# Kernel tuning notes

Measured on AMD Instinct MI355X. Metric: run time of the kernel, lower is better.

The kernel has to match this reference:

```python
import jax, jax.numpy as jnp
import numpy as np

MAX_PATH_DISTANCE = 5


def setup_inputs() -> dict:
    key = jax.random.key(0)
    k1, k2, k3, k4, k5 = jax.random.split(key, 5)
    N = 8192
    E = 4_000_000
    x = jax.random.normal(k1, (N, 128), dtype=jnp.float32)
    src = jax.random.randint(k2, (E,), 0, N, dtype=jnp.int64)
    dst = jax.random.randint(k3, (E,), 0, N, dtype=jnp.int64)
    # path lengths; original computes len(paths[src][dst]) >= 1
    path_len = jax.random.randint(k4, (E,), 0, 6, dtype=jnp.int64)
    # learned parameter b of shape [max_path_distance]
    b = jax.random.normal(k5, (MAX_PATH_DISTANCE,), dtype=jnp.float32)
    return {"x": x, "b": b, "src": src, "dst": dst, "path_len": path_len}


def reference(x, b, src, dst, path_len):
    N = x.shape[0]
    # index = min(len, max_path_distance) - 1, clamped to valid range
    idx = jnp.clip(path_len, 1, MAX_PATH_DISTANCE) - 1  # [E]
    vals = b[idx]  # [E] gather from tiny table
    spatial = jnp.zeros((N, N), dtype=b.dtype)
    spatial = spatial.at[src, dst].set(vals)  # scatter into pairwise bias matrix
    return spatial
```

## Files before the change

kernel.cpp:

```cpp
#include <hip/hip_runtime.h>

#define MAX_PATH_DISTANCE 5
#define NROW 8192
#define ROWS_PER_BKT 128
#define NBKT 64
#define SLICES 17
#define EPB 4096
#define CAPB (SLICES * EPB)
#define CAPR 768
#define BLK 512
#define NWAVE 8
#define NHG 4
#define EPT 8


__device__ __forceinline__ int clamp_bidx(int pl) {
    int c = pl < 1 ? 1 : (pl > MAX_PATH_DISTANCE ? MAX_PATH_DISTANCE : pl);
    return c - 1;
}

__global__ __launch_bounds__(BLK) void se_coarse(
        const int4* __restrict__ src4, const int4* __restrict__ dst4,
        const int4* __restrict__ plen4,
        unsigned long long* __restrict__ bkt,
        unsigned int* __restrict__ bkt_cur, int E4) {
    __shared__ __align__(16) unsigned long long stage[EPB];
    __shared__ unsigned int hist[NWAVE][NBKT], wb[NWAVE][NBKT];
    __shared__ unsigned int base_l[NBKT], gbase[NBKT], s_total;
    const int tid = threadIdx.x;
    const int w   = tid >> 6;
    const int q0  = blockIdx.x * (EPB / 4);

    for (int i = tid; i < NWAVE * NBKT; i += BLK) (&hist[0][0])[i] = 0u;
    __syncthreads();

    unsigned long long ent[EPT];
#pragma unroll
    for (int g = 0; g < 2; ++g) {
        int q = q0 + g * BLK + tid;
        if (q < E4) {
            int4 s = src4[q], d = dst4[q], p = plen4[q];
            int ss[4] = {s.x, s.y, s.z, s.w};
            int dd[4] = {d.x, d.y, d.z, d.w};
            int pp[4] = {p.x, p.y, p.z, p.w};
#pragma unroll
            for (int c = 0; c < 4; ++c) {
                int e = (q << 2) + c;
                unsigned int key = ((unsigned int)(e + 1) << 3)
                                 | (unsigned int)clamp_bidx(pp[c]);
                unsigned long long v =
                      ((unsigned long long)(unsigned int)ss[c] << 38)
                    | ((unsigned long long)(unsigned int)dd[c] << 25)
                    | (unsigned long long)key;
                ent[g * 4 + c] = v;
                atomicAdd(&hist[w][(unsigned int)(v >> 45)], 1u);
            }
        } else {
#pragma unroll
            for (int c = 0; c < 4; ++c) ent[g * 4 + c] = 0ull;
        }
    }
    __syncthreads();

    if (tid < NBKT) {
        unsigned int t = 0;
#pragma unroll
        for (int ww = 0; ww < NWAVE; ++ww) t += hist[ww][tid];
        base_l[tid] = t;
    }
    __syncthreads();
    if (tid == 0) {
        unsigned int run = 0;
        for (int i = 0; i < NBKT; ++i) {
            unsigned int t = base_l[i]; base_l[i] = run; run += t;
        }
        s_total = run;
    }
    __syncthreads();
    if (tid < NBKT) {
        unsigned int t = base_l[tid], tot = 0;
#pragma unroll
        for (int ww = 0; ww < NWAVE; ++ww) {
            wb[ww][tid] = t; t += hist[ww][tid]; tot += hist[ww][tid];
        }
        gbase[tid] = atomicAdd(&bkt_cur[tid], tot);
    }
    __syncthreads();

#pragma unroll
    for (int j = 0; j < EPT; ++j) {
        if (ent[j]) {
            unsigned int bb = (unsigned int)(ent[j] >> 45);
            unsigned int p  = atomicAdd(&wb[w][bb], 1u);
            stage[p] = ent[j];
        }
    }
    __syncthreads();

    const unsigned int total = s_total;
    for (unsigned int i = tid; i < total; i += BLK) {
        unsigned long long v = stage[i];
        unsigned int bb  = (unsigned int)(v >> 45);
        unsigned int pos = gbase[bb] + (i - base_l[bb]);
        if (pos < CAPB) bkt[(size_t)bb * CAPB + pos] = v;
    }
}

__global__ __launch_bounds__(BLK) void se_fine(
        const unsigned long long* __restrict__ bkt,
        const unsigned int* __restrict__ bkt_cur,
        unsigned long long* __restrict__ rbins,
        unsigned int* __restrict__ rcur) {
    __shared__ __align__(16) unsigned long long stage[EPB];
    __shared__ unsigned int hist[NHG][ROWS_PER_BKT];
    __shared__ unsigned int wb[NHG][ROWS_PER_BKT];
    __shared__ unsigned int base_l[ROWS_PER_BKT], gbase[ROWS_PER_BKT], s_total;
    const int tid = threadIdx.x;
    const int w   = tid >> 7;
    const int b   = blockIdx.x / SLICES;
    const int sl  = blockIdx.x % SLICES;

    unsigned int cnt = bkt_cur[b]; if (cnt > CAPB) cnt = CAPB;
    const int i0 = sl * EPB;
    int n = (int)cnt - i0;
    if (n <= 0) return;
    if (n > EPB) n = EPB;

    for (int i = tid; i < NHG * ROWS_PER_BKT; i += BLK) (&hist[0][0])[i] = 0u;
    __syncthreads();

    const unsigned long long* bp = bkt + (size_t)b * CAPB + i0;
    unsigned long long ent[EPT];
#pragma unroll
    for (int j = 0; j < EPT; ++j) {
        int i = j * BLK + tid;
        ent[j] = 0ull;
        if (i < n) {
            ent[j] = bp[i];
            atomicAdd(&hist[w][(unsigned int)(ent[j] >> 38) & 127u], 1u);
        }
    }
    __syncthreads();

    if (tid < ROWS_PER_BKT) {
        unsigned int t = 0;
#pragma unroll
        for (int ww = 0; ww < NHG; ++ww) t += hist[ww][tid];
        base_l[tid] = t;
    }
    __syncthreads();
    if (tid == 0) {
        unsigned int run = 0;
        for (int i = 0; i < ROWS_PER_BKT; ++i) {
            unsigned int t = base_l[i]; base_l[i] = run; run += t;
        }
        s_total = run;
    }
    __syncthreads();
    if (tid < ROWS_PER_BKT) {
        unsigned int t = base_l[tid], tot = 0;
#pragma unroll
        for (int ww = 0; ww < NHG; ++ww) {
            wb[ww][tid] = t; t += hist[ww][tid]; tot += hist[ww][tid];
        }
        gbase[tid] = atomicAdd(&rcur[b * ROWS_PER_BKT + tid], tot);
    }
    __syncthreads();

#pragma unroll
    for (int j = 0; j < EPT; ++j) {
        if (ent[j]) {
            unsigned int rl = (unsigned int)(ent[j] >> 38) & 127u;
            unsigned int p  = atomicAdd(&wb[w][rl], 1u);
            stage[p] = ent[j];
        }
    }
    __syncthreads();

    const unsigned int total = s_total;
    for (unsigned int i = tid; i < total; i += BLK) {
        unsigned long long v = stage[i];
        unsigned int s   = (unsigned int)((v >> 38) & 0x1FFFu);
        unsigned int rl  = s & 127u;
        unsigned int pos = gbase[rl] + (i - base_l[rl]);
        if (pos < CAPR) rbins[(size_t)s * CAPR + pos] = v;
    }
}

__global__ __launch_bounds__(BLK) void se_rows(
        const unsigned long long* __restrict__ rbins,
        const unsigned int* __restrict__ rcur,
        const float* __restrict__ bias,
        float* __restrict__ out) {
    __shared__ unsigned int lds[NROW];
    const int tid = threadIdx.x;
    const int r0  = blockIdx.x * 2;

    unsigned int cntA = rcur[r0];     if (cntA > CAPR) cntA = CAPR;
    unsigned int cntB = rcur[r0 + 1]; if (cntB > CAPR) cntB = CAPR;
    const unsigned long long* bpA = rbins + (size_t)r0 * CAPR;
    const unsigned long long* bpB = bpA + CAPR;

    unsigned long long a0 = 0ull, a1 = 0ull, b0 = 0ull, b1 = 0ull;
    if ((unsigned int)tid < cntA)        a0 = bpA[tid];
    if ((unsigned int)tid + BLK < cntA)  a1 = bpA[tid + BLK];
    if ((unsigned int)tid < cntB)        b0 = bpB[tid];
    if ((unsigned int)tid + BLK < cntB)  b1 = bpB[tid + BLK];

    for (int i = tid; i < NROW; i += BLK) lds[i] = 0u;
    __syncthreads();
    if (a0) atomicMax(&lds[(unsigned int)((a0 >> 25) & 0x1FFFu)],
                      (unsigned int)(a0 & 0x1FFFFFFu));
    if (a1) atomicMax(&lds[(unsigned int)((a1 >> 25) & 0x1FFFu)],
                      (unsigned int)(a1 & 0x1FFFFFFu));
    __syncthreads();
    if (a0) {
        unsigned int key = (unsigned int)(a0 & 0x1FFFFFFu);
        unsigned int d   = (unsigned int)((a0 >> 25) & 0x1FFFu);
        if (lds[d] == key) lds[d] = __float_as_uint(bias[key & 7u]);
    }
    if (a1) {
        unsigned int key = (unsigned int)(a1 & 0x1FFFFFFu);
        unsigned int d   = (unsigned int)((a1 >> 25) & 0x1FFFu);
        if (lds[d] == key) lds[d] = __float_as_uint(bias[key & 7u]);
    }
    __syncthreads();
    {
        float4* out4 = reinterpret_cast<float4*>(out + (size_t)r0 * NROW);
        const float4* l4 = reinterpret_cast<const float4*>(lds);
#pragma unroll
        for (int k = 0; k < NROW / 4 / BLK; ++k)
            out4[k * BLK + tid] = l4[k * BLK + tid];
    }
    __syncthreads();

    for (int i = tid; i < NROW; i += BLK) lds[i] = 0u;
    __syncthreads();
    if (b0) atomicMax(&lds[(unsigned int)((b0 >> 25) & 0x1FFFu)],
                      (unsigned int)(b0 & 0x1FFFFFFu));
    if (b1) atomicMax(&lds[(unsigned int)((b1 >> 25) & 0x1FFFu)],
                      (unsigned int)(b1 & 0x1FFFFFFu));
    __syncthreads();
    if (b0) {
        unsigned int key = (unsigned int)(b0 & 0x1FFFFFFu);
        unsigned int d   = (unsigned int)((b0 >> 25) & 0x1FFFu);
        if (lds[d] == key) lds[d] = __float_as_uint(bias[key & 7u]);
    }
    if (b1) {
        unsigned int key = (unsigned int)(b1 & 0x1FFFFFFu);
        unsigned int d   = (unsigned int)((b1 >> 25) & 0x1FFFu);
        if (lds[d] == key) lds[d] = __float_as_uint(bias[key & 7u]);
    }
    __syncthreads();
    {
        float4* out4 = reinterpret_cast<float4*>(out + (size_t)(r0 + 1) * NROW);
        const float4* l4 = reinterpret_cast<const float4*>(lds);
#pragma unroll
        for (int k = 0; k < NROW / 4 / BLK; ++k)
            out4[k * BLK + tid] = l4[k * BLK + tid];
    }
}


__global__ void se_scatter_keys(const int* __restrict__ src,
                                const int* __restrict__ dst,
                                const int* __restrict__ plen,
                                unsigned int* __restrict__ out,
                                int E, int N) {
    int e = blockIdx.x * blockDim.x + threadIdx.x;
    if (e >= E) return;
    unsigned int key = ((unsigned int)(e + 1) << 3)
                     | (unsigned int)clamp_bidx(plen[e]);
    atomicMax(&out[(size_t)src[e] * (size_t)N + (size_t)dst[e]], key);
}

__global__ void se_resolve(const int* __restrict__ src,
                           const int* __restrict__ dst,
                           const int* __restrict__ plen,
                           const float* __restrict__ b,
                           unsigned int* __restrict__ out,
                           int E, int N) {
    int e = blockIdx.x * blockDim.x + threadIdx.x;
    if (e >= E) return;
    unsigned int key = ((unsigned int)(e + 1) << 3)
                     | (unsigned int)clamp_bidx(plen[e]);
    size_t off = (size_t)src[e] * (size_t)N + (size_t)dst[e];
    if (out[off] == key) {
        reinterpret_cast<float*>(out)[off] = b[key & 7u];
    }
}


extern "C" void kernel_launch(void* const* d_in, const int* in_sizes, int n_in,
                              void* d_out, int out_size, void* d_ws, size_t ws_size,
                              hipStream_t stream) {
    const float* b    = (const float*)d_in[1];
    const int*   src  = (const int*)d_in[2];
    const int*   dst  = (const int*)d_in[3];
    const int*   plen = (const int*)d_in[4];

    const int N = in_sizes[0] / 128;
    const int E = in_sizes[2];

    const size_t rbins_bytes = (size_t)NROW * CAPR * sizeof(unsigned long long);
    const size_t bkt_bytes   = (size_t)NBKT * CAPB * sizeof(unsigned long long);
    const size_t cur_bytes   = (size_t)(NROW + NBKT) * sizeof(unsigned int);
    const size_t need = rbins_bytes + bkt_bytes + cur_bytes;

    if (N == NROW && (unsigned int)E < (1u << 22) && (E % 4) == 0 &&
        ws_size >= need) {
        unsigned long long* rbins = (unsigned long long*)d_ws;
        unsigned long long* bktp  = (unsigned long long*)((char*)d_ws + rbins_bytes);
        unsigned int* rcur = (unsigned int*)((char*)d_ws + rbins_bytes + bkt_bytes);
        unsigned int* bcur = rcur + NROW;

        hipMemsetAsync(rcur, 0, cur_bytes, stream);
        se_coarse<<<(E + EPB - 1) / EPB, BLK, 0, stream>>>(
            (const int4*)src, (const int4*)dst, (const int4*)plen,
            bktp, bcur, E / 4);
        se_fine<<<NBKT * SLICES, BLK, 0, stream>>>(bktp, bcur, rbins, rcur);
        se_rows<<<NROW / 2, BLK, 0, stream>>>(rbins, rcur, b, (float*)d_out);
    } else {
        const int block = 256;
        const int gridE = (E + block - 1) / block;
        hipMemsetAsync(d_out, 0, (size_t)out_size * sizeof(float), stream);
        se_scatter_keys<<<gridE, block, 0, stream>>>(src, dst, plen,
                                                     (unsigned int*)d_out, E, N);
        se_resolve<<<gridE, block, 0, stream>>>(src, dst, plen, b,
                                                (unsigned int*)d_out, E, N);
    }
}
```

Baseline: 107.9 us.

## Replace LDS atomic histograms with wave-level ballot match ranking and shuffle scans

In both the coarse and fine bucketing kernels, per-element LDS atomicAdds for the histogram and the scatter pass are replaced by a ballot-based match: lanes in a wave with the same bucket are grouped, ranked by popcount, and one leader lane updates the per-wave counter. The single-thread serial prefix sum over buckets becomes a wave shuffle scan. The fine kernel moves from 4 to 8 per-wave histogram groups. This removes LDS atomic contention and a serial scan, but adds 6–7 ballots per element, which could cost more when buckets rarely match within a wave.

```diff
diff --git a/kernel.cpp b/kernel.cpp
--- a/kernel.cpp
+++ b/kernel.cpp
@@ -10,13 +10,24 @@
 #define CAPR 768
 #define BLK 512
 #define NWAVE 8
-#define NHG 4
 #define EPT 8
 
 
 __device__ __forceinline__ int clamp_bidx(int pl) {
     int c = pl < 1 ? 1 : (pl > MAX_PATH_DISTANCE ? MAX_PATH_DISTANCE : pl);
     return c - 1;
+}
+
+template <int NBITS>
+__device__ __forceinline__ unsigned long long same_mask(unsigned int b,
+                                                        unsigned long long valid) {
+    unsigned long long same = valid;
+#pragma unroll
+    for (int k = 0; k < NBITS; ++k) {
+        unsigned long long m = __ballot((b >> k) & 1u);
+        same &= ((b >> k) & 1u) ? m : ~m;
+    }
+    return same;
 }
 
 __global__ __launch_bounds__(BLK) void se_coarse(
@@ -25,11 +36,14 @@
         unsigned long long* __restrict__ bkt,
         unsigned int* __restrict__ bkt_cur, int E4) {
     __shared__ __align__(16) unsigned long long stage[EPB];
-    __shared__ unsigned int hist[NWAVE][NBKT], wb[NWAVE][NBKT];
-    __shared__ unsigned int base_l[NBKT], gbase[NBKT], s_total;
-    const int tid = threadIdx.x;
-    const int w   = tid >> 6;
-    const int q0  = blockIdx.x * (EPB / 4);
+    __shared__ unsigned int hist[NWAVE][NBKT];
+    __shared__ unsigned int base_l[NBKT], cnt_col[NBKT], gbase[NBKT];
+    __shared__ unsigned int s_total;
+    const int tid  = threadIdx.x;
+    const int w    = tid >> 6;
+    const int lane = tid & 63;
+    const unsigned long long lane_lt = ((unsigned long long)1 << lane) - 1ull;
+    const int q0 = blockIdx.x * (EPB / 4);
 
     for (int i = tid; i < NWAVE * NBKT; i += BLK) (&hist[0][0])[i] = 0u;
     __syncthreads();
@@ -48,51 +62,70 @@
                 int e = (q << 2) + c;
                 unsigned int key = ((unsigned int)(e + 1) << 3)
                                  | (unsigned int)clamp_bidx(pp[c]);
-                unsigned long long v =
+                ent[g * 4 + c] =
                       ((unsigned long long)(unsigned int)ss[c] << 38)
                     | ((unsigned long long)(unsigned int)dd[c] << 25)
                     | (unsigned long long)key;
-                ent[g * 4 + c] = v;
-                atomicAdd(&hist[w][(unsigned int)(v >> 45)], 1u);
             }
         } else {
 #pragma unroll
             for (int c = 0; c < 4; ++c) ent[g * 4 + c] = 0ull;
         }
     }
+
+    unsigned int pb[EPT];
+#pragma unroll
+    for (int j = 0; j < EPT; ++j) {
+        unsigned int b = (unsigned int)(ent[j] >> 45);
+        bool vld = ent[j] != 0ull;
+        unsigned long long valid = __ballot(vld);
+        unsigned long long same  = same_mask<6>(b, valid);
+        unsigned int rank = __popcll(same & lane_lt);
+        int ldr1 = __ffsll((long long)same);
+        unsigned int cnt = __popcll(same);
+        unsigned int base_v = 0;
+        if (vld && lane == ldr1 - 1) {
+            base_v = hist[w][b];
+            hist[w][b] = base_v + cnt;
+        }
+        base_v = __shfl(base_v, ldr1 > 0 ? ldr1 - 1 : 0, 64);
+        pb[j] = base_v + rank;
+    }
     __syncthreads();
 
     if (tid < NBKT) {
         unsigned int t = 0;
 #pragma unroll
         for (int ww = 0; ww < NWAVE; ++ww) t += hist[ww][tid];
-        base_l[tid] = t;
-    }
-    __syncthreads();
-    if (tid == 0) {
-        unsigned int run = 0;
-        for (int i = 0; i < NBKT; ++i) {
-            unsigned int t = base_l[i]; base_l[i] = run; run += t;
-        }
-        s_total = run;
+        cnt_col[tid] = t;
+    }
+    __syncthreads();
+    if (tid < 64) {
+        unsigned int v = cnt_col[tid], inc = v;
+#pragma unroll
+        for (int off = 1; off < 64; off <<= 1) {
+            unsigned int y = __shfl_up(inc, off, 64);
+            if (lane >= off) inc += y;
+        }
+        base_l[tid] = inc - v;
+        if (tid == 63) s_total = inc;
+        gbase[tid] = atomicAdd(&bkt_cur[tid], v);
     }
     __syncthreads();
     if (tid < NBKT) {
-        unsigned int t = base_l[tid], tot = 0;
+        unsigned int t = base_l[tid];
 #pragma unroll
         for (int ww = 0; ww < NWAVE; ++ww) {
-            wb[ww][tid] = t; t += hist[ww][tid]; tot += hist[ww][tid];
-        }
-        gbase[tid] = atomicAdd(&bkt_cur[tid], tot);
+            unsigned int o = hist[ww][tid]; hist[ww][tid] = t; t += o;
+        }
     }
     __syncthreads();
 
 #pragma unroll
     for (int j = 0; j < EPT; ++j) {
         if (ent[j]) {
-            unsigned int bb = (unsigned int)(ent[j] >> 45);
-            unsigned int p  = atomicAdd(&wb[w][bb], 1u);
-            stage[p] = ent[j];
+            unsigned int b = (unsigned int)(ent[j] >> 45);
+            stage[hist[w][b] + pb[j]] = ent[j];
         }
     }
     __syncthreads();
@@ -112,21 +145,24 @@
         unsigned long long* __restrict__ rbins,
         unsigned int* __restrict__ rcur) {
     __shared__ __align__(16) unsigned long long stage[EPB];
-    __shared__ unsigned int hist[NHG][ROWS_PER_BKT];
-    __shared__ unsigned int wb[NHG][ROWS_PER_BKT];
-    __shared__ unsigned int base_l[ROWS_PER_BKT], gbase[ROWS_PER_BKT], s_total;
-    const int tid = threadIdx.x;
-    const int w   = tid >> 7;
-    const int b   = blockIdx.x / SLICES;
-    const int sl  = blockIdx.x % SLICES;
-
-    unsigned int cnt = bkt_cur[b]; if (cnt > CAPB) cnt = CAPB;
+    __shared__ unsigned int hist[NWAVE][ROWS_PER_BKT];
+    __shared__ unsigned int base_l[ROWS_PER_BKT], cnt_col[ROWS_PER_BKT],
+                            gbase[ROWS_PER_BKT];
+    __shared__ unsigned int s_total;
+    const int tid  = threadIdx.x;
+    const int w    = tid >> 6;
+    const int lane = tid & 63;
+    const unsigned long long lane_lt = ((unsigned long long)1 << lane) - 1ull;
+    const int b  = blockIdx.x / SLICES;
+    const int sl = blockIdx.x % SLICES;
+
+    unsigned int cnt0 = bkt_cur[b]; if (cnt0 > CAPB) cnt0 = CAPB;
     const int i0 = sl * EPB;
-    int n = (int)cnt - i0;
+    int n = (int)cnt0 - i0;
     if (n <= 0) return;
     if (n > EPB) n = EPB;
 
-    for (int i = tid; i < NHG * ROWS_PER_BKT; i += BLK) (&hist[0][0])[i] = 0u;
+    for (int i = tid; i < NWAVE * ROWS_PER_BKT; i += BLK) (&hist[0][0])[i] = 0u;
     __syncthreads();
 
     const unsigned long long* bp = bkt + (size_t)b * CAPB + i0;
@@ -134,36 +170,58 @@
 #pragma unroll
     for (int j = 0; j < EPT; ++j) {
         int i = j * BLK + tid;
-        ent[j] = 0ull;
-        if (i < n) {
-            ent[j] = bp[i];
-            atomicAdd(&hist[w][(unsigned int)(ent[j] >> 38) & 127u], 1u);
-        }
+        ent[j] = (i < n) ? bp[i] : 0ull;
+    }
+
+    unsigned int pb[EPT];
+#pragma unroll
+    for (int j = 0; j < EPT; ++j) {
+        unsigned int rl = (unsigned int)(ent[j] >> 38) & 127u;
+        bool vld = ent[j] != 0ull;
+        unsigned long long valid = __ballot(vld);
+        unsigned long long same  = same_mask<7>(rl, valid);
+        unsigned int rank = __popcll(same & lane_lt);
+        int ldr1 = __ffsll((long long)same);
+        unsigned int cnt = __popcll(same);
+        unsigned int base_v = 0;
+        if (vld && lane == ldr1 - 1) {
+            base_v = hist[w][rl];
+            hist[w][rl] = base_v + cnt;
+        }
+        base_v = __shfl(base_v, ldr1 > 0 ? ldr1 - 1 : 0, 64);
+        pb[j] = base_v + rank;
     }
     __syncthreads();
 
     if (tid < ROWS_PER_BKT) {
         unsigned int t = 0;
 #pragma unroll
-        for (int ww = 0; ww < NHG; ++ww) t += hist[ww][tid];
-        base_l[tid] = t;
-    }
-    __syncthreads();
-    if (tid == 0) {
-        unsigned int run = 0;
-        for (int i = 0; i < ROWS_PER_BKT; ++i) {
-            unsigned int t = base_l[i]; base_l[i] = run; run += t;
-        }
-        s_total = run;
+        for (int ww = 0; ww < NWAVE; ++ww) t += hist[ww][tid];
+        cnt_col[tid] = t;
+    }
+    __syncthreads();
+    if (tid < 64) {
+        unsigned int a  = cnt_col[tid], c2 = cnt_col[tid + 64];
+        unsigned int ia = a, ib = c2;
+#pragma unroll
+        for (int off = 1; off < 64; off <<= 1) {
+            unsigned int ya = __shfl_up(ia, off, 64);
+            unsigned int yb = __shfl_up(ib, off, 64);
+            if (lane >= off) { ia += ya; ib += yb; }
+        }
+        unsigned int totA = __shfl(ia, 63, 64);
+        base_l[tid]      = ia - a;
+        base_l[tid + 64] = totA + ib - c2;
+        if (tid == 63) s_total = totA + ib;
     }
     __syncthreads();
     if (tid < ROWS_PER_BKT) {
-        unsigned int t = base_l[tid], tot = 0;
-#pragma unroll
-        for (int ww = 0; ww < NHG; ++ww) {
-            wb[ww][tid] = t; t += hist[ww][tid]; tot += hist[ww][tid];
-        }
-        gbase[tid] = atomicAdd(&rcur[b * ROWS_PER_BKT + tid], tot);
+        gbase[tid] = atomicAdd(&rcur[b * ROWS_PER_BKT + tid], cnt_col[tid]);
+        unsigned int t = base_l[tid];
+#pragma unroll
+        for (int ww = 0; ww < NWAVE; ++ww) {
+            unsigned int o = hist[ww][tid]; hist[ww][tid] = t; t += o;
+        }
     }
     __syncthreads();
 
@@ -171,8 +229,7 @@
     for (int j = 0; j < EPT; ++j) {
         if (ent[j]) {
             unsigned int rl = (unsigned int)(ent[j] >> 38) & 127u;
-            unsigned int p  = atomicAdd(&wb[w][rl], 1u);
-            stage[p] = ent[j];
+            stage[hist[w][rl] + pb[j]] = ent[j];
         }
     }
     __syncthreads();
```

Result: slower. 111.8 us (+3.6%).
